# Optimization experiments

Hardware: AMD Instinct MI355X
Metric: run time of the kernel (lower is better)

## Reference

```python
import jax, jax.numpy as jnp
import numpy as np
import math

N_QUBITS = 8
N_LAYERS = 4
DIM = 2 ** N_QUBITS


def _ry(theta):
    # theta: (...,) -> (..., 2, 2) real RY matrix, cast to complex64
    c, s = jnp.cos(theta / 2), jnp.sin(theta / 2)
    g = jnp.stack([jnp.stack([c, -s], -1), jnp.stack([s, c], -1)], -2)
    return g.astype(jnp.complex64)


def _apply_1q(psi, gate, q):
    # psi: (B, 2**n); gate: (2,2) shared or (B,2,2) per-sample; qubit q (wire 0 = MSB)
    B = psi.shape[0]
    L, R = 2 ** q, 2 ** (N_QUBITS - q - 1)
    s = psi.reshape(B, L, 2, R)
    if gate.ndim == 2:
        s = jnp.einsum('ij,bljr->blir', gate, s)
    else:
        s = jnp.einsum('bij,bljr->blir', gate, s)
    return s.reshape(B, DIM)


def _cnot(psi, c):
    # CNOT on adjacent wires (c, c+1): swap |10> <-> |11> on that 4-dim block
    B = psi.shape[0]
    L, R = 2 ** c, 2 ** (N_QUBITS - c - 2)
    s = psi.reshape(B, L, 4, R)
    s = s[:, :, jnp.array([0, 1, 3, 2]), :]
    return s.reshape(B, DIM)


def setup_inputs() -> dict:
    key = jax.random.key(0)
    kx, kw = jax.random.split(key)
    B = 65536
    x = jax.random.uniform(kx, (B, N_QUBITS), jnp.float32, -math.pi, math.pi)
    bound = 1.0 / math.sqrt(N_QUBITS)
    weights = jax.random.uniform(kw, (N_LAYERS, N_QUBITS, 2), jnp.float32, -bound, bound)
    return {"x": x, "weights": weights}


def reference(x, weights):
    B = x.shape[0]
    # |0...0> initial state
    psi = jnp.zeros((B, DIM), jnp.complex64).at[:, 0].set(1.0)
    # angle encoding: RY(x_i) on wire i (per-sample gates)
    enc = _ry(x)  # (B, n, 2, 2)
    for q in range(N_QUBITS):
        psi = _apply_1q(psi, enc[:, q], q)
    # variational layers: RY(w[l,i,0]) then RZ(w[l,i,1]) on each wire, then CNOT chain
    for l in range(N_LAYERS):
        ry = _ry(weights[l, :, 0])  # (n, 2, 2)
        tz = weights[l, :, 1]
        ez_m = jnp.exp(-0.5j * tz.astype(jnp.complex64))  # e^{-i theta/2}
        ez_p = jnp.exp(0.5j * tz.astype(jnp.complex64))   # e^{+i theta/2}
        phases = jnp.stack([ez_m, ez_p], axis=-1)  # (n, 2) diag of RZ
        g = phases[:, :, None] * ry  # (n,2,2) = RZ @ RY (fused rotation)
        for q in range(N_QUBITS):
            psi = _apply_1q(psi, g[q], q)
        for c in range(N_QUBITS - 1):
            psi = _cnot(psi, c)
    # PauliZ expectations per wire
    p = psi.real ** 2 + psi.imag ** 2  # (B, DIM)
    exps = []
    for q in range(N_QUBITS):
        pq = p.reshape(B, 2 ** q, 2, -1).sum(axis=(1, 3))  # (B, 2)
        exps.append(pq[:, 0] - pq[:, 1])
    return jnp.stack(exps, axis=1)  # (B, n_qubits)
```

## Files before the change

kernel.cpp:

```cpp
#include <hip/hip_runtime.h>


typedef _Float16 half8  __attribute__((ext_vector_type(8)));
typedef float    float4v __attribute__((ext_vector_type(4)));
typedef unsigned int uint2v __attribute__((ext_vector_type(2)));

#define PBASE 4096
#define WAVE_LDS 12288

#define MEMFENCE() __asm__ volatile("" ::: "memory")

__device__ __forceinline__ unsigned pk2(float a, float b) {
  auto v = __builtin_amdgcn_cvt_pkrtz(a, b);
  return __builtin_bit_cast(unsigned, v);
}
__device__ __forceinline__ float rdlane(float v, int l) {
  return __builtin_bit_cast(float, __builtin_amdgcn_readlane(__builtin_bit_cast(int, v), l));
}

__launch_bounds__(256, 2)
__global__ void qmain(const float* __restrict__ x, const float* __restrict__ w,
                      float* __restrict__ out) {
  __shared__ __align__(16) unsigned char smem[4 * WAVE_LDS];
  const int tid = threadIdx.x;
  const int lane = tid & 63, wv = tid >> 6;
  const int quad = lane >> 4, n = lane & 15;
  unsigned char* sm = smem + wv * WAVE_LDS;

  {
    const int t = wv;
    int mr = n ^ ((n >> 1) & 1);
    mr ^= ((mr >> 2) & 1) << 1;
    mr ^= ((mr >> 3) & 1) << 2;
    float cS[8], sS[8], zcS[8], zsS[8];
#pragma unroll
    for (int qq = 0; qq < 8; ++qq) {
      float th = w[(t * 8 + qq) * 2 + 0];
      float tz = w[(t * 8 + qq) * 2 + 1];
      __sincosf(0.5f * th, &sS[qq], &cS[qq]);
      __sincosf(0.5f * tz, &zsS[qq], &zcS[qq]);
    }
    union { _Float16 h[8]; half8 v; } aR, aI, bR, bI;
#pragma unroll
    for (int ci = 0; ci < 4; ++ci) {
      const int col = quad * 4 + ci;
      float hr = 1.f, hi = 0.f;
#pragma unroll
      for (int qq = 0; qq < 4; ++qq) {
        int rb = (mr >> (3 - qq)) & 1, cb = (col >> (3 - qq)) & 1;
        float ryv = (rb == cb) ? cS[qq] : (rb ? sS[qq] : -sS[qq]);
        float ar = zcS[qq] * ryv;
        float ai = (rb ? zsS[qq] : -zsS[qq]) * ryv;
        float nr = hr * ar - hi * ai, ni = hr * ai + hi * ar;
        hr = nr; hi = ni;
      }
      aR.h[2 * ci + 0] = (_Float16)hr;
      aR.h[2 * ci + 1] = (_Float16)(-hi);
      aI.h[2 * ci + 0] = (_Float16)hi;
      aI.h[2 * ci + 1] = (_Float16)hr;
      float wr = 1.f, wi = 0.f;
#pragma unroll
      for (int qq = 0; qq < 4; ++qq) {
        int rb = (n >> (3 - qq)) & 1, cb = (col >> (3 - qq)) & 1;
        float ryv = (rb == cb) ? cS[qq + 4] : (rb ? sS[qq + 4] : -sS[qq + 4]);
        float ar = zcS[qq + 4] * ryv;
        float ai = (rb ? zsS[qq + 4] : -zsS[qq + 4]) * ryv;
        float nr = wr * ar - wi * ai, ni = wr * ai + wi * ar;
        wr = nr; wi = ni;
      }
      bR.h[2 * ci + 0] = (_Float16)wr;
      bR.h[2 * ci + 1] = (_Float16)(-wi);
      bI.h[2 * ci + 0] = (_Float16)wi;
      bI.h[2 * ci + 1] = (_Float16)wr;
    }
    half8* FB = (half8*)smem;
    FB[(t * 4 + 0) * 64 + lane] = aR.v;
    FB[(t * 4 + 1) * 64 + lane] = aI.v;
    FB[(t * 4 + 2) * 64 + lane] = bR.v;
    FB[(t * 4 + 3) * 64 + lane] = bI.v;
  }
  __syncthreads();
  half8 aLR[4], aLI[4], aRR[4], aRI[4];
#pragma unroll
  for (int t = 0; t < 4; ++t) {
    const half8* FB = (const half8*)smem;
    aLR[t] = FB[(t * 4 + 0) * 64 + lane];
    aLI[t] = FB[(t * 4 + 1) * 64 + lane];
    aRR[t] = FB[(t * 4 + 2) * 64 + lane];
    aRI[t] = FB[(t * 4 + 3) * 64 + lane];
  }
  __syncthreads();

  unsigned wS[4], wP[4];
#pragma unroll
  for (int r = 0; r < 4; ++r) {
    int L = quad * 4 + r;
    wS[r] = (unsigned)(L * 128 + (((n >> 2) ^ (L & 7)) << 4) + (n & 3) * 4);
    int y = L ^ ((n & 1) << 3);
    y ^= ((y >> 3) & 1) << 2;
    y ^= ((y >> 2) & 1) << 1;
    y ^= (y >> 1) & 1;
    wP[r] = (unsigned)(y * 128 + (((n >> 2) ^ (y & 7)) << 4) + (n & 3) * 4);
  }
  const unsigned rS = (unsigned)(n * 128 + ((quad ^ (n & 7)) << 4));
  const unsigned pWg = (unsigned)(2 * n + (quad >> 1));
  const unsigned pWlo = (unsigned)(PBASE + (quad & 1) * 8);

  unsigned char* smA = sm;
  unsigned char* smB = sm + 2048;
  const int e0 = (blockIdx.x * 4 + wv) * 32;
  const float4v zz = {0.f, 0.f, 0.f, 0.f};

  for (int g = 0; g < 2; ++g) {
    const int base = e0 + g * 16;
    float xa = x[(size_t)base * 8 + lane];
    float xb = x[(size_t)base * 8 + 64 + lane];
    float ca, sa, cb, sb;
    __sincosf(0.5f * xa, &sa, &ca);
    __sincosf(0.5f * xb, &sb, &cb);

    for (int i = 0; i < 8; ++i) {
      half8 bv[2];
#pragma unroll
      for (int h = 0; h < 2; ++h) {
        const int e = 2 * i + h;
        const float cs = (i < 4) ? ca : cb;
        const float sn = (i < 4) ? sa : sb;
        const int lb = (e & 7) * 8;
        float cq[8], sq[8];
#pragma unroll
        for (int q = 0; q < 8; ++q) {
          cq[q] = rdlane(cs, lb + q);
          sq[q] = rdlane(sn, lb + q);
        }
        float f0 = (quad & 2) ? sq[0] : cq[0];
        float f1 = (quad & 1) ? sq[1] : cq[1];
        float f4 = (n & 8) ? sq[4] : cq[4];
        float f5 = (n & 4) ? sq[5] : cq[5];
        float f6 = (n & 2) ? sq[6] : cq[6];
        float f7 = (n & 1) ? sq[7] : cq[7];
        float pb = f0 * f1 * f4 * f5 * f6 * f7;
        float v0 = pb * cq[2] * cq[3], v1 = pb * cq[2] * sq[3];
        float v2 = pb * sq[2] * cq[3], v3 = pb * sq[2] * sq[3];
        union { unsigned u[4]; half8 v; } bb;
        bb.u[0] = pk2(v0, 0.f); bb.u[1] = pk2(v1, 0.f);
        bb.u[2] = pk2(v2, 0.f); bb.u[3] = pk2(v3, 0.f);
        bv[h] = bb.v;
      }

      half8 bA = bv[0], bB = bv[1];
      const unsigned eA = (unsigned)(2 * i), eB = eA + 1u;
      const unsigned pA = pWlo + eA * 512u + ((pWg ^ (eA & 7u)) << 4);
      const unsigned pB = pWlo + eB * 512u + ((pWg ^ (eB & 7u)) << 4);
#pragma unroll
      for (int t = 0; t < 4; ++t) {
        if (t) {
          MEMFENCE();
          bA = *(const half8*)(smA + rS);
          bB = *(const half8*)(smB + rS);
        }
        float4v xrA = __builtin_amdgcn_mfma_f32_16x16x32_f16(aLR[t], bA, zz, 0, 0, 0);
        float4v xiA = __builtin_amdgcn_mfma_f32_16x16x32_f16(aLI[t], bA, zz, 0, 0, 0);
        float4v xrB = __builtin_amdgcn_mfma_f32_16x16x32_f16(aLR[t], bB, zz, 0, 0, 0);
        float4v xiB = __builtin_amdgcn_mfma_f32_16x16x32_f16(aLI[t], bB, zz, 0, 0, 0);
        MEMFENCE();
#pragma unroll
        for (int r = 0; r < 4; ++r) {
          *(unsigned*)(smA + wS[r]) = pk2(xrA[r], xiA[r]);
          *(unsigned*)(smB + wS[r]) = pk2(xrB[r], xiB[r]);
        }
        MEMFENCE();
        half8 cA = *(const half8*)(smA + rS);
        half8 cB = *(const half8*)(smB + rS);
        float4v yrA = __builtin_amdgcn_mfma_f32_16x16x32_f16(aRR[t], cA, zz, 0, 0, 0);
        float4v yiA = __builtin_amdgcn_mfma_f32_16x16x32_f16(aRI[t], cA, zz, 0, 0, 0);
        float4v yrB = __builtin_amdgcn_mfma_f32_16x16x32_f16(aRR[t], cB, zz, 0, 0, 0);
        float4v yiB = __builtin_amdgcn_mfma_f32_16x16x32_f16(aRI[t], cB, zz, 0, 0, 0);
        MEMFENCE();
        if (t < 3) {
#pragma unroll
          for (int r = 0; r < 4; ++r) {
            *(unsigned*)(smA + wP[r]) = pk2(yrA[r], yiA[r]);
            *(unsigned*)(smB + wP[r]) = pk2(yrB[r], yiB[r]);
          }
        } else {
          float a0 = yrA[0] * yrA[0] + yiA[0] * yiA[0];
          float a1 = yrA[1] * yrA[1] + yiA[1] * yiA[1];
          float a2 = yrA[2] * yrA[2] + yiA[2] * yiA[2];
          float a3 = yrA[3] * yrA[3] + yiA[3] * yiA[3];
          uint2v pvA = { pk2(a0, a1), pk2(a2, a3) };
          *(uint2v*)(sm + pA) = pvA;
          float b0 = yrB[0] * yrB[0] + yiB[0] * yiB[0];
          float b1 = yrB[1] * yrB[1] + yiB[1] * yiB[1];
          float b2 = yrB[2] * yrB[2] + yiB[2] * yiB[2];
          float b3 = yrB[3] * yrB[3] + yiB[3] * yiB[3];
          uint2v pvB = { pk2(b0, b1), pk2(b2, b3) };
          *(uint2v*)(sm + pB) = pvB;
        }
      }
    }

    float4v acc = zz;
    MEMFENCE();
#pragma unroll
    for (int c = 0; c < 8; ++c) {
      union { _Float16 h[8]; half8 v; } sg;
#pragma unroll
      for (int j = 0; j < 8; ++j) {
        int u = 2 * c + (quad >> 1);
        int lp = (quad & 1) * 8 + j;
        int y = lp ^ ((u & 1) << 3);
        y ^= ((y >> 3) & 1) << 2;
        y ^= ((y >> 2) & 1) << 1;
        y ^= (y >> 1) & 1;
        float sv = 0.f;
        if (n < 8) {
          int bit = (n < 4) ? ((u >> (3 - n)) & 1) : ((y >> (7 - n)) & 1);
          sv = bit ? -1.f : 1.f;
        }
        sg.h[j] = (_Float16)sv;
      }
      unsigned pR = (unsigned)(PBASE + n * 512 +
                               ((((unsigned)(c * 4 + quad)) ^ (unsigned)(n & 7)) << 4));
      half8 pbv = *(const half8*)(sm + pR);
      acc = __builtin_amdgcn_mfma_f32_16x16x32_f16(sg.v, pbv, acc, 0, 0, 0);
    }
    MEMFENCE();
    if (quad < 2) {
      float4v* o = (float4v*)(out + (size_t)(base + n) * 8 + quad * 4);
      *o = acc;
    }
  }
}

extern "C" void kernel_launch(void* const* d_in, const int* in_sizes, int n_in,
                              void* d_out, int out_size, void* d_ws, size_t ws_size,
                              hipStream_t stream) {
  const float* x = (const float*)d_in[0];
  const float* w = (const float*)d_in[1];
  float* out = (float*)d_out;
  qmain<<<dim3(512), dim3(256), 0, stream>>>(x, w, out);
}
```

Baseline: 84.36 us.

## Keep state in registers between MFMAs using transposed operands and DPP swaps

Swaps the MFMA operand roles so the state is the A operand and the gate matrices are the B operand. The output of one MFMA can then be packed directly into the input of the next, which removes the LDS write/read round trips between the left and right gate applications and between layers. The CNOT permutation is folded into the gate construction, together with a row_ror-style DPP lane swap. The sign matrix for the final expectation reduction is also precomputed once instead of per group, and the per-wave LDS shrinks to hold only the probability buffer. The risk is correctness of the remapped permutation and the added DPP instructions in the dependent chain.

Result: faster. 79.49 us (-5.8%).

```diff
diff --git a/kernel.cpp b/kernel.cpp
--- a/kernel.cpp
+++ b/kernel.cpp
@@ -4,9 +4,7 @@
 typedef _Float16 half8  __attribute__((ext_vector_type(8)));
 typedef float    float4v __attribute__((ext_vector_type(4)));
 typedef unsigned int uint2v __attribute__((ext_vector_type(2)));
-
-#define PBASE 4096
-#define WAVE_LDS 12288
+typedef unsigned int uint4v __attribute__((ext_vector_type(4)));
 
 #define MEMFENCE() __asm__ volatile("" ::: "memory")
 
@@ -17,15 +15,27 @@
 __device__ __forceinline__ float rdlane(float v, int l) {
   return __builtin_bit_cast(float, __builtin_amdgcn_readlane(__builtin_bit_cast(int, v), l));
 }
+__device__ __forceinline__ unsigned sw8u(unsigned v) {
+  return (unsigned)__builtin_amdgcn_mov_dpp((int)v, 0x128, 0xf, 0xf, false);
+}
+__device__ __forceinline__ float sw8f(float v) {
+  return __builtin_bit_cast(float,
+      __builtin_amdgcn_mov_dpp(__builtin_bit_cast(int, v), 0x128, 0xf, 0xf, false));
+}
+__device__ __forceinline__ int tauf(int l) {
+  int y = l ^ (((l >> 3) & 1) << 2);
+  y ^= ((y >> 2) & 1) << 1;
+  y ^= (y >> 1) & 1;
+  return y;
+}
 
 __launch_bounds__(256, 2)
 __global__ void qmain(const float* __restrict__ x, const float* __restrict__ w,
                       float* __restrict__ out) {
-  __shared__ __align__(16) unsigned char smem[4 * WAVE_LDS];
+  __shared__ __align__(16) unsigned char smem[32768];
   const int tid = threadIdx.x;
   const int lane = tid & 63, wv = tid >> 6;
   const int quad = lane >> 4, n = lane & 15;
-  unsigned char* sm = smem + wv * WAVE_LDS;
 
   {
     const int t = wv;
@@ -40,76 +50,78 @@
       __sincosf(0.5f * th, &sS[qq], &cS[qq]);
       __sincosf(0.5f * tz, &zsS[qq], &zcS[qq]);
     }
-    union { _Float16 h[8]; half8 v; } aR, aI, bR, bI;
+    union { _Float16 h[8]; half8 v; } bLR, bLI, bRR, bRI;
 #pragma unroll
     for (int ci = 0; ci < 4; ++ci) {
-      const int col = quad * 4 + ci;
+      const int kp = quad * 4 + ci;
       float hr = 1.f, hi = 0.f;
 #pragma unroll
-      for (int qq = 0; qq < 4; ++qq) {
-        int rb = (mr >> (3 - qq)) & 1, cb = (col >> (3 - qq)) & 1;
-        float ryv = (rb == cb) ? cS[qq] : (rb ? sS[qq] : -sS[qq]);
-        float ar = zcS[qq] * ryv;
-        float ai = (rb ? zsS[qq] : -zsS[qq]) * ryv;
+      for (int j = 0; j < 4; ++j) {
+        int rb = (mr >> (3 - j)) & 1, cb = (kp >> (3 - j)) & 1;
+        float ryv = (rb == cb) ? cS[j] : (rb ? sS[j] : -sS[j]);
+        float ar = zcS[j] * ryv;
+        float ai = (rb ? zsS[j] : -zsS[j]) * ryv;
         float nr = hr * ar - hi * ai, ni = hr * ai + hi * ar;
         hr = nr; hi = ni;
       }
-      aR.h[2 * ci + 0] = (_Float16)hr;
-      aR.h[2 * ci + 1] = (_Float16)(-hi);
-      aI.h[2 * ci + 0] = (_Float16)hi;
-      aI.h[2 * ci + 1] = (_Float16)hr;
+      bLR.h[2 * ci] = (_Float16)hr;  bLR.h[2 * ci + 1] = (_Float16)(-hi);
+      bLI.h[2 * ci] = (_Float16)hi;  bLI.h[2 * ci + 1] = (_Float16)hr;
+      int yk = tauf(kp);
       float wr = 1.f, wi = 0.f;
 #pragma unroll
-      for (int qq = 0; qq < 4; ++qq) {
-        int rb = (n >> (3 - qq)) & 1, cb = (col >> (3 - qq)) & 1;
-        float ryv = (rb == cb) ? cS[qq + 4] : (rb ? sS[qq + 4] : -sS[qq + 4]);
-        float ar = zcS[qq + 4] * ryv;
-        float ai = (rb ? zsS[qq + 4] : -zsS[qq + 4]) * ryv;
+      for (int j = 0; j < 4; ++j) {
+        int rb = (n >> (3 - j)) & 1, cb = (yk >> (3 - j)) & 1;
+        float ryv = (rb == cb) ? cS[4 + j] : (rb ? sS[4 + j] : -sS[4 + j]);
+        float ar = zcS[4 + j] * ryv;
+        float ai = (rb ? zsS[4 + j] : -zsS[4 + j]) * ryv;
         float nr = wr * ar - wi * ai, ni = wr * ai + wi * ar;
         wr = nr; wi = ni;
       }
-      bR.h[2 * ci + 0] = (_Float16)wr;
-      bR.h[2 * ci + 1] = (_Float16)(-wi);
-      bI.h[2 * ci + 0] = (_Float16)wi;
-      bI.h[2 * ci + 1] = (_Float16)wr;
+      bRR.h[2 * ci] = (_Float16)wr;  bRR.h[2 * ci + 1] = (_Float16)(-wi);
+      bRI.h[2 * ci] = (_Float16)wi;  bRI.h[2 * ci + 1] = (_Float16)wr;
     }
     half8* FB = (half8*)smem;
-    FB[(t * 4 + 0) * 64 + lane] = aR.v;
-    FB[(t * 4 + 1) * 64 + lane] = aI.v;
-    FB[(t * 4 + 2) * 64 + lane] = bR.v;
-    FB[(t * 4 + 3) * 64 + lane] = bI.v;
+    FB[(t * 4 + 0) * 64 + lane] = bLR.v;
+    FB[(t * 4 + 1) * 64 + lane] = bLI.v;
+    FB[(t * 4 + 2) * 64 + lane] = bRR.v;
+    FB[(t * 4 + 3) * 64 + lane] = bRI.v;
   }
   __syncthreads();
-  half8 aLR[4], aLI[4], aRR[4], aRI[4];
+  half8 BLR[4], BLI[4], BRR[4], BRI[4];
 #pragma unroll
   for (int t = 0; t < 4; ++t) {
     const half8* FB = (const half8*)smem;
-    aLR[t] = FB[(t * 4 + 0) * 64 + lane];
-    aLI[t] = FB[(t * 4 + 1) * 64 + lane];
-    aRR[t] = FB[(t * 4 + 2) * 64 + lane];
-    aRI[t] = FB[(t * 4 + 3) * 64 + lane];
+    BLR[t] = FB[(t * 4 + 0) * 64 + lane];
+    BLI[t] = FB[(t * 4 + 1) * 64 + lane];
+    BRR[t] = FB[(t * 4 + 2) * 64 + lane];
+    BRI[t] = FB[(t * 4 + 3) * 64 + lane];
   }
   __syncthreads();
 
-  unsigned wS[4], wP[4];
-#pragma unroll
-  for (int r = 0; r < 4; ++r) {
-    int L = quad * 4 + r;
-    wS[r] = (unsigned)(L * 128 + (((n >> 2) ^ (L & 7)) << 4) + (n & 3) * 4);
-    int y = L ^ ((n & 1) << 3);
-    y ^= ((y >> 3) & 1) << 2;
-    y ^= ((y >> 2) & 1) << 1;
-    y ^= (y >> 1) & 1;
-    wP[r] = (unsigned)(y * 128 + (((n >> 2) ^ (y & 7)) << 4) + (n & 3) * 4);
-  }
-  const unsigned rS = (unsigned)(n * 128 + ((quad ^ (n & 7)) << 4));
+  half8 sf[8];
+#pragma unroll
+  for (int c = 0; c < 8; ++c) {
+    union { _Float16 h[8]; half8 v; } sg;
+#pragma unroll
+    for (int jj = 0; jj < 8; ++jj) {
+      int u = (quad & 1) * 8 + jj;
+      int y = tauf(2 * c + (quad >> 1));
+      float sv = 0.f;
+      if (n < 8) {
+        int bit = (n < 4) ? ((u >> (3 - n)) & 1) : ((y >> (7 - n)) & 1);
+        sv = bit ? -1.f : 1.f;
+      }
+      sg.h[jj] = (_Float16)sv;
+    }
+    sf[c] = sg.v;
+  }
+
+  unsigned char* smp = smem + wv * 8192;
   const unsigned pWg = (unsigned)(2 * n + (quad >> 1));
-  const unsigned pWlo = (unsigned)(PBASE + (quad & 1) * 8);
-
-  unsigned char* smA = sm;
-  unsigned char* smB = sm + 2048;
+  const unsigned pWlo = (unsigned)((quad & 1) * 8);
   const int e0 = (blockIdx.x * 4 + wv) * 32;
   const float4v zz = {0.f, 0.f, 0.f, 0.f};
+  const int ytau = tauf(n);
 
   for (int g = 0; g < 2; ++g) {
     const int base = e0 + g * 16;
@@ -120,7 +132,7 @@
     __sincosf(0.5f * xb, &sb, &cb);
 
     for (int i = 0; i < 8; ++i) {
-      half8 bv[2];
+      uint4v st[2];
 #pragma unroll
       for (int h = 0; h < 2; ++h) {
         const int e = 2 * i + h;
@@ -129,73 +141,69 @@
         const int lb = (e & 7) * 8;
         float cq[8], sq[8];
 #pragma unroll
-        for (int q = 0; q < 8; ++q) {
-          cq[q] = rdlane(cs, lb + q);
-          sq[q] = rdlane(sn, lb + q);
-        }
+        for (int q = 0; q < 8; ++q) { cq[q] = rdlane(cs, lb + q); sq[q] = rdlane(sn, lb + q); }
         float f0 = (quad & 2) ? sq[0] : cq[0];
         float f1 = (quad & 1) ? sq[1] : cq[1];
-        float f4 = (n & 8) ? sq[4] : cq[4];
-        float f5 = (n & 4) ? sq[5] : cq[5];
-        float f6 = (n & 2) ? sq[6] : cq[6];
-        float f7 = (n & 1) ? sq[7] : cq[7];
+        float f4 = (ytau & 8) ? sq[4] : cq[4];
+        float f5 = (ytau & 4) ? sq[5] : cq[5];
+        float f6 = (ytau & 2) ? sq[6] : cq[6];
+        float f7 = (ytau & 1) ? sq[7] : cq[7];
         float pb = f0 * f1 * f4 * f5 * f6 * f7;
-        float v0 = pb * cq[2] * cq[3], v1 = pb * cq[2] * sq[3];
-        float v2 = pb * sq[2] * cq[3], v3 = pb * sq[2] * sq[3];
-        union { unsigned u[4]; half8 v; } bb;
-        bb.u[0] = pk2(v0, 0.f); bb.u[1] = pk2(v1, 0.f);
-        bb.u[2] = pk2(v2, 0.f); bb.u[3] = pk2(v3, 0.f);
-        bv[h] = bb.v;
-      }
-
-      half8 bA = bv[0], bB = bv[1];
-      const unsigned eA = (unsigned)(2 * i), eB = eA + 1u;
-      const unsigned pA = pWlo + eA * 512u + ((pWg ^ (eA & 7u)) << 4);
-      const unsigned pB = pWlo + eB * 512u + ((pWg ^ (eB & 7u)) << 4);
+        st[h][0] = pk2(pb * cq[2] * cq[3], 0.f);
+        st[h][1] = pk2(pb * cq[2] * sq[3], 0.f);
+        st[h][2] = pk2(pb * sq[2] * cq[3], 0.f);
+        st[h][3] = pk2(pb * sq[2] * sq[3], 0.f);
+      }
+
 #pragma unroll
       for (int t = 0; t < 4; ++t) {
-        if (t) {
+        half8 A0 = __builtin_bit_cast(half8, st[0]);
+        half8 A1 = __builtin_bit_cast(half8, st[1]);
+        float4v xr0 = __builtin_amdgcn_mfma_f32_16x16x32_f16(A0, BLR[t], zz, 0, 0, 0);
+        float4v xi0 = __builtin_amdgcn_mfma_f32_16x16x32_f16(A0, BLI[t], zz, 0, 0, 0);
+        float4v xr1 = __builtin_amdgcn_mfma_f32_16x16x32_f16(A1, BLR[t], zz, 0, 0, 0);
+        float4v xi1 = __builtin_amdgcn_mfma_f32_16x16x32_f16(A1, BLI[t], zz, 0, 0, 0);
+        uint4v X0 = { pk2(xr0[0], xi0[0]), pk2(xr0[1], xi0[1]),
+                      pk2(xr0[2], xi0[2]), pk2(xr0[3], xi0[3]) };
+        uint4v X1 = { pk2(xr1[0], xi1[0]), pk2(xr1[1], xi1[1]),
+                      pk2(xr1[2], xi1[2]), pk2(xr1[3], xi1[3]) };
+        half8 XA0 = __builtin_bit_cast(half8, X0);
+        half8 XA1 = __builtin_bit_cast(half8, X1);
+        float4v yr0 = __builtin_amdgcn_mfma_f32_16x16x32_f16(XA0, BRR[t], zz, 0, 0, 0);
+        float4v yi0 = __builtin_amdgcn_mfma_f32_16x16x32_f16(XA0, BRI[t], zz, 0, 0, 0);
+        float4v yr1 = __builtin_amdgcn_mfma_f32_16x16x32_f16(XA1, BRR[t], zz, 0, 0, 0);
+        float4v yi1 = __builtin_amdgcn_mfma_f32_16x16x32_f16(XA1, BRI[t], zz, 0, 0, 0);
+        if (t < 3) {
+          st[0][0] = pk2(yr0[0], yi0[0]);
+          st[0][1] = sw8u(pk2(yr0[1], yi0[1]));
+          st[0][2] = pk2(yr0[2], yi0[2]);
+          st[0][3] = sw8u(pk2(yr0[3], yi0[3]));
+          st[1][0] = pk2(yr1[0], yi1[0]);
+          st[1][1] = sw8u(pk2(yr1[1], yi1[1]));
+          st[1][2] = pk2(yr1[2], yi1[2]);
+          st[1][3] = sw8u(pk2(yr1[3], yi1[3]));
+        } else {
+          float r01 = sw8f(yr0[1]), i01 = sw8f(yi0[1]);
+          float r03 = sw8f(yr0[3]), i03 = sw8f(yi0[3]);
+          float p00 = yr0[0] * yr0[0] + yi0[0] * yi0[0];
+          float p01 = r01 * r01 + i01 * i01;
+          float p02 = yr0[2] * yr0[2] + yi0[2] * yi0[2];
+          float p03 = r03 * r03 + i03 * i03;
+          float r11 = sw8f(yr1[1]), i11 = sw8f(yi1[1]);
+          float r13 = sw8f(yr1[3]), i13 = sw8f(yi1[3]);
+          float p10 = yr1[0] * yr1[0] + yi1[0] * yi1[0];
+          float p11 = r11 * r11 + i11 * i11;
+          float p12 = yr1[2] * yr1[2] + yi1[2] * yi1[2];
+          float p13 = r13 * r13 + i13 * i13;
+          const unsigned eA = (unsigned)(2 * i), eB = eA + 1u;
+          unsigned pA = eA * 512u + ((pWg ^ (eA & 7u)) << 4) + pWlo;
+          unsigned pB = eB * 512u + ((pWg ^ (eB & 7u)) << 4) + pWlo;
           MEMFENCE();
-          bA = *(const half8*)(smA + rS);
-          bB = *(const half8*)(smB + rS);
-        }
-        float4v xrA = __builtin_amdgcn_mfma_f32_16x16x32_f16(aLR[t], bA, zz, 0, 0, 0);
-        float4v xiA = __builtin_amdgcn_mfma_f32_16x16x32_f16(aLI[t], bA, zz, 0, 0, 0);
-        float4v xrB = __builtin_amdgcn_mfma_f32_16x16x32_f16(aLR[t], bB, zz, 0, 0, 0);
-        float4v xiB = __builtin_amdgcn_mfma_f32_16x16x32_f16(aLI[t], bB, zz, 0, 0, 0);
-        MEMFENCE();
-#pragma unroll
-        for (int r = 0; r < 4; ++r) {
-          *(unsigned*)(smA + wS[r]) = pk2(xrA[r], xiA[r]);
-          *(unsigned*)(smB + wS[r]) = pk2(xrB[r], xiB[r]);
-        }
-        MEMFENCE();
-        half8 cA = *(const half8*)(smA + rS);
-        half8 cB = *(const half8*)(smB + rS);
-        float4v yrA = __builtin_amdgcn_mfma_f32_16x16x32_f16(aRR[t], cA, zz, 0, 0, 0);
-        float4v yiA = __builtin_amdgcn_mfma_f32_16x16x32_f16(aRI[t], cA, zz, 0, 0, 0);
-        float4v yrB = __builtin_amdgcn_mfma_f32_16x16x32_f16(aRR[t], cB, zz, 0, 0, 0);
-        float4v yiB = __builtin_amdgcn_mfma_f32_16x16x32_f16(aRI[t], cB, zz, 0, 0, 0);
-        MEMFENCE();
-        if (t < 3) {
-#pragma unroll
-          for (int r = 0; r < 4; ++r) {
-            *(unsigned*)(smA + wP[r]) = pk2(yrA[r], yiA[r]);
-            *(unsigned*)(smB + wP[r]) = pk2(yrB[r], yiB[r]);
-          }
-        } else {
-          float a0 = yrA[0] * yrA[0] + yiA[0] * yiA[0];
-          float a1 = yrA[1] * yrA[1] + yiA[1] * yiA[1];
-          float a2 = yrA[2] * yrA[2] + yiA[2] * yiA[2];
-          float a3 = yrA[3] * yrA[3] + yiA[3] * yiA[3];
-          uint2v pvA = { pk2(a0, a1), pk2(a2, a3) };
-          *(uint2v*)(sm + pA) = pvA;
-          float b0 = yrB[0] * yrB[0] + yiB[0] * yiB[0];
-          float b1 = yrB[1] * yrB[1] + yiB[1] * yiB[1];
-          float b2 = yrB[2] * yrB[2] + yiB[2] * yiB[2];
-          float b3 = yrB[3] * yrB[3] + yiB[3] * yiB[3];
-          uint2v pvB = { pk2(b0, b1), pk2(b2, b3) };
-          *(uint2v*)(sm + pB) = pvB;
+          uint2v v0 = { pk2(p00, p01), pk2(p02, p03) };
+          *(uint2v*)(smp + pA) = v0;
+          uint2v v1 = { pk2(p10, p11), pk2(p12, p13) };
+          *(uint2v*)(smp + pB) = v1;
+          MEMFENCE();
         }
       }
     }
@@ -204,26 +212,10 @@
     MEMFENCE();
 #pragma unroll
     for (int c = 0; c < 8; ++c) {
-      union { _Float16 h[8]; half8 v; } sg;
-#pragma unroll
-      for (int j = 0; j < 8; ++j) {
-        int u = 2 * c + (quad >> 1);
-        int lp = (quad & 1) * 8 + j;
-        int y = lp ^ ((u & 1) << 3);
-        y ^= ((y >> 3) & 1) << 2;
-        y ^= ((y >> 2) & 1) << 1;
-        y ^= (y >> 1) & 1;
-        float sv = 0.f;
-        if (n < 8) {
-          int bit = (n < 4) ? ((u >> (3 - n)) & 1) : ((y >> (7 - n)) & 1);
-          sv = bit ? -1.f : 1.f;
-        }
-        sg.h[j] = (_Float16)sv;
-      }
-      unsigned pR = (unsigned)(PBASE + n * 512 +
+      unsigned pR = (unsigned)(n * 512 +
                                ((((unsigned)(c * 4 + quad)) ^ (unsigned)(n & 7)) << 4));
-      half8 pbv = *(const half8*)(sm + pR);
-      acc = __builtin_amdgcn_mfma_f32_16x16x32_f16(sg.v, pbv, acc, 0, 0, 0);
+      half8 pbv = *(const half8*)(smp + pR);
+      acc = __builtin_amdgcn_mfma_f32_16x16x32_f16(sf[c], pbv, acc, 0, 0, 0);
     }
     MEMFENCE();
     if (quad < 2) {
```
